# Optimization experiments

Measured on AMD Instinct MI355X. Metric: run time of the kernel, lower is better.

Reference implementation:

```python
import jax, jax.numpy as jnp
import numpy as np

H = 8        # hidden_size
T = 609      # seq_size
IN = 5       # input feature dim
B = 2048     # batch


def _lstm_layer(x, Wih, Whh, bih, bhh):
    """PyTorch-compatible single-layer LSTM, batch_first. x: [B, T, I].
    Gate order i, f, g, o; zero initial (h, c)."""
    b = x.shape[0]
    h_dim = Wih.shape[0] // 4
    bias = bih + bhh

    def step(carry, xt):
        h, c = carry
        gates = xt @ Wih.T + h @ Whh.T + bias          # [B, 4H]
        i, f, g, o = jnp.split(gates, 4, axis=-1)
        i = jax.nn.sigmoid(i)
        f = jax.nn.sigmoid(f)
        g = jnp.tanh(g)
        o = jax.nn.sigmoid(o)
        c = f * c + i * g
        h = o * jnp.tanh(c)
        return (h, c), h

    h0 = jnp.zeros((b, h_dim), x.dtype)
    (_, _), ys = jax.lax.scan(step, (h0, h0), jnp.swapaxes(x, 0, 1))  # ys: [T, B, H]
    return jnp.swapaxes(ys, 0, 1)                                      # [B, T, H]


def setup_inputs() -> dict:
    key = jax.random.key(0)
    ks = jax.random.split(key, 20)
    s_lstm = 1.0 / np.sqrt(H)   # PyTorch LSTM init scale

    def u(k, shape, s):
        return jax.random.uniform(k, shape, jnp.float32, -s, s)

    inp = {"x": jax.random.normal(ks[0], (B, T, IN), jnp.float32)}
    # LSTM layer 1 (input 5), layers 2-3 (input H)
    ins = [IN, H, H]
    for l in range(3):
        k0, k1, k2, k3 = jax.random.split(ks[1 + l], 4)
        inp[f"Wih{l+1}"] = u(k0, (4 * H, ins[l]), s_lstm)
        inp[f"Whh{l+1}"] = u(k1, (4 * H, H), s_lstm)
        inp[f"bih{l+1}"] = u(k2, (4 * H,), s_lstm)
        inp[f"bhh{l+1}"] = u(k3, (4 * H,), s_lstm)
    # MLP head
    d_in = H * T  # 4872
    dims = [(4096, d_in), (1024, 4096), (T, 1024)]
    for i, (o, ii) in enumerate(dims):
        s = 1.0 / np.sqrt(ii)
        k0, k1 = jax.random.split(ks[10 + i], 2)
        inp[f"W{i+1}"] = u(k0, (o, ii), s)
        inp[f"b{i+1}"] = u(k1, (o,), s)
    return inp


def reference(x, Wih1, Whh1, bih1, bhh1, Wih2, Whh2, bih2, bhh2,
              Wih3, Whh3, bih3, bhh3, W1, b1, W2, b2, W3, b3):
    out = _lstm_layer(x, Wih1, Whh1, bih1, bhh1)
    out = _lstm_layer(out, Wih2, Whh2, bih2, bhh2)
    out = _lstm_layer(out, Wih3, Whh3, bih3, bhh3)
    out = out.reshape(x.shape[0], -1)              # [B, T*H]
    out = jax.nn.relu(out @ W1.T + b1)
    out = jax.nn.relu(out @ W2.T + b2)
    out = out @ W3.T + b3                          # [B, T]
    return out
```

## Files before the change

kernel.cpp:

```cpp
#include <hip/hip_runtime.h>
#include <hip/hip_bf16.h>

typedef __attribute__((ext_vector_type(8))) short short8;
typedef __attribute__((ext_vector_type(4))) float floatx4;
typedef unsigned short u16;

#define T_SZ 609
#define K1V  4872
#define K1P  4928
#define RD   4

static __device__ __forceinline__ u16 f2bf(float f) {
    union { float f; unsigned u; } a; a.f = f;
    unsigned r = a.u + 0x7FFF + ((a.u >> 16) & 1);
    return (u16)(r >> 16);
}

static __device__ __forceinline__ void gload_lds16(const u16* g, u16* l) {
    __builtin_amdgcn_global_load_lds(
        (const __attribute__((address_space(1))) void*)g,
        (__attribute__((address_space(3))) void*)l, 16, 0, 0);
}

#define WG_LOAD(p)     __hip_atomic_load((p), __ATOMIC_ACQUIRE, __HIP_MEMORY_SCOPE_WORKGROUP)
#define WG_STORE(p, v) __hip_atomic_store((p), (v), __ATOMIC_RELEASE, __HIP_MEMORY_SCOPE_WORKGROUP)

static __device__ __forceinline__ void cvt8(const float* __restrict__ p, u16* __restrict__ d) {
    float4 a = *(const float4*)p;
    float4 b = *(const float4*)(p + 4);
    u16 o[8] = { f2bf(a.x), f2bf(a.y), f2bf(a.z), f2bf(a.w),
                 f2bf(b.x), f2bf(b.y), f2bf(b.z), f2bf(b.w) };
    *(uint4*)d = *(const uint4*)o;
}
static __device__ __forceinline__ void zero8(u16* __restrict__ d) {
    *(uint4*)d = (uint4){0, 0, 0, 0};
}

__global__ __launch_bounds__(192) void lstm3_fused(
    const float* __restrict__ x,
    const float* __restrict__ Wih1, const float* __restrict__ Whh1,
    const float* __restrict__ bih1, const float* __restrict__ bhh1,
    const float* __restrict__ Wih2, const float* __restrict__ Whh2,
    const float* __restrict__ bih2, const float* __restrict__ bhh2,
    const float* __restrict__ Wih3, const float* __restrict__ Whh3,
    const float* __restrict__ bih3, const float* __restrict__ bhh3,
    u16* __restrict__ A1,
    const float* __restrict__ W1, u16* __restrict__ W1b,
    const float* __restrict__ W2, u16* __restrict__ W2b,
    const float* __restrict__ W3, u16* __restrict__ W3b)
{
    if (blockIdx.x >= 1024) {
        const int ct = (blockIdx.x - 1024) * 192 + threadIdx.x;
        const int cs = 256 * 192;
        for (int i = ct; i < 4096 * 616; i += cs) {
            int r = i / 616, c = (i - r * 616) << 3;
            u16* d = W1b + (size_t)r * K1P + c;
            if (c < K1V) cvt8(W1 + (size_t)r * K1V + c, d); else zero8(d);
        }
        for (int i = ct; i < 524288; i += cs)
            cvt8(W2 + (size_t)i * 8, W2b + (size_t)i * 8);
        for (int i = ct; i < 640 * 128; i += cs) {
            int r = i >> 7, c = (i & 127) << 3;
            u16* d = W3b + (size_t)r * 1024 + c;
            if (r < T_SZ) cvt8(W3 + (size_t)r * 1024 + c, d); else zero8(d);
        }
        return;
    }

    __shared__ __align__(16) float xs[2 * T_SZ * 5];
    __shared__ __align__(16) float r1[RD * 16], r2[RD * 16], r3[RD * 16];
    __shared__ int p1, p2, c2, c3;

    const int tid = threadIdx.x;
    const int b0  = blockIdx.x * 2;

    const float* xg = x + (size_t)b0 * (T_SZ * 5);
    for (int i = tid; i < 2 * T_SZ * 5; i += 192) xs[i] = xg[i];
    if (tid == 0) { p1 = 0; p2 = 0; c2 = 0; c3 = 0; }
    if (tid < 112) {
        int r = tid / 56, c = tid - r * 56;
        A1[(size_t)(b0 + r) * K1P + K1V + c] = 0;
    }
    __syncthreads();

    const int lane = tid & 63, wid = tid >> 6;
    const int gi   = lane & 31;
    const int rh   = lane >> 5;
    const int jj   = gi & 7;
    const int gt   = gi >> 3;
    const int base = lane & 32;

    const float am = (gt == 2) ? -2.f : -1.f;
    const float aa = (gt == 2) ?  2.f :  1.f;
    const float ab = (gt == 2) ? -1.f :  0.f;

    auto lstep = [&](float a, float& c) -> float {
        float e = __expf(am * a);
        float v = __builtin_fmaf(aa, __fdividef(1.f, 1.f + e), ab);
        float vi = __shfl(v, base + jj,      64);
        float vf = __shfl(v, base + 8 + jj,  64);
        float vg = __shfl(v, base + 16 + jj, 64);
        float vo = __shfl(v, base + 24 + jj, 64);
        c = __builtin_fmaf(vf, c, vi * vg);
        float ec = __expf(-2.f * __builtin_fabsf(c));
        float th = (1.f - ec) * __fdividef(1.f, 1.f + ec);
        return vo * __builtin_copysignf(th, c);
    };

    auto dot8 = [&](const float* hp, const float* w, float& a, float& b) {
        float4 h0 = *(const float4*)hp;
        float4 h1 = *(const float4*)(hp + 4);
        a = __builtin_fmaf(w[0], h0.x, a); b = __builtin_fmaf(w[1], h0.y, b);
        a = __builtin_fmaf(w[2], h0.z, a); b = __builtin_fmaf(w[3], h0.w, b);
        a = __builtin_fmaf(w[4], h1.x, a); b = __builtin_fmaf(w[5], h1.y, b);
        a = __builtin_fmaf(w[6], h1.z, a); b = __builtin_fmaf(w[7], h1.w, b);
    };

    if (wid == 0) {
        float wi[5], wh[8];
#pragma unroll
        for (int k = 0; k < 5; ++k) wi[k] = Wih1[gi * 5 + k];
#pragma unroll
        for (int k = 0; k < 8; ++k) wh[k] = Whh1[gi * 8 + k];
        const float bs = bih1[gi] + bhh1[gi];
        const float* xr = &xs[rh * (T_SZ * 5)];
        float cst = 0.f;
        for (int t = 0; t < T_SZ; ++t) {
            float a = bs, b = 0.f;
#pragma unroll
            for (int k = 0; k < 5; ++k) a = __builtin_fmaf(wi[k], xr[t * 5 + k], a);
            if (t > 0) dot8(&r1[((t - 1) & (RD - 1)) * 16 + rh * 8], wh, a, b);
            float h = lstep(a + b, cst);
            if (t >= RD) while (WG_LOAD(&c2) < t - (RD - 1)) {}
            if (gi < 8) r1[(t & (RD - 1)) * 16 + rh * 8 + jj] = h;
            if (lane == 0) WG_STORE(&p1, t + 1);
        }
    } else if (wid == 1) {
        float wi[8], wh[8];
#pragma unroll
        for (int k = 0; k < 8; ++k) { wi[k] = Wih2[gi * 8 + k]; wh[k] = Whh2[gi * 8 + k]; }
        const float bs = bih2[gi] + bhh2[gi];
        float cst = 0.f;
        for (int t = 0; t < T_SZ; ++t) {
            while (WG_LOAD(&p1) < t + 1) {}
            float a = bs, b = 0.f;
            dot8(&r1[(t & (RD - 1)) * 16 + rh * 8], wi, a, b);
            if (lane == 0) WG_STORE(&c2, t + 1);
            if (t > 0) dot8(&r2[((t - 1) & (RD - 1)) * 16 + rh * 8], wh, a, b);
            float h = lstep(a + b, cst);
            if (t >= RD) while (WG_LOAD(&c3) < t - (RD - 1)) {}
            if (gi < 8) r2[(t & (RD - 1)) * 16 + rh * 8 + jj] = h;
            if (lane == 0) WG_STORE(&p2, t + 1);
        }
    } else {
        float wi[8], wh[8];
#pragma unroll
        for (int k = 0; k < 8; ++k) { wi[k] = Wih3[gi * 8 + k]; wh[k] = Whh3[gi * 8 + k]; }
        const float bs = bih3[gi] + bhh3[gi];
        float cst = 0.f;
        u16* outp = A1 + (size_t)(b0 + rh) * K1P;
        for (int t = 0; t < T_SZ; ++t) {
            while (WG_LOAD(&p2) < t + 1) {}
            float a = bs, b = 0.f;
            dot8(&r2[(t & (RD - 1)) * 16 + rh * 8], wi, a, b);
            if (lane == 0) WG_STORE(&c3, t + 1);
            if (t > 0) dot8(&r3[((t - 1) & (RD - 1)) * 16 + rh * 8], wh, a, b);
            float h = lstep(a + b, cst);
            if (gi < 8) {
                r3[(t & (RD - 1)) * 16 + rh * 8 + jj] = h;
                outp[t * 8 + jj] = f2bf(h);
            }
        }
    }
}

template<int BM, int BN, bool RELU, bool NGUARD, bool OUTF32>
__global__ __launch_bounds__(256) void gemm_bt(
    const u16* __restrict__ A, int lda,
    const u16* __restrict__ B, int ldb,
    const float* __restrict__ bias,
    void* __restrict__ Cv, int ldc, int N, int K)
{
    constexpr int WM = BM / 2, WN = BN / 2;
    constexpr int TM = WM / 16, TN = WN / 16;
    __shared__ u16 As[BM * 64];
    __shared__ u16 Bs[BN * 64];

    const int tid = threadIdx.x;
    const int bm  = blockIdx.y * BM;
    const int bn  = blockIdx.x * BN;
    const int l   = tid & 63, w = tid >> 6;
    const int wr  = w >> 1, wc = w & 1;
    const int lr  = l & 15, q = l >> 4;
    const int lrow = l >> 3;
    const int lcol = (l & 7) << 3;

    floatx4 acc[TM][TN];
#pragma unroll
    for (int i = 0; i < TM; ++i)
#pragma unroll
        for (int j = 0; j < TN; ++j) acc[i][j] = (floatx4){0.f, 0.f, 0.f, 0.f};

    const u16* Ab = A + (size_t)bm * lda;
    const u16* Bb = B + (size_t)bn * ldb;

    for (int k0 = 0; k0 < K; k0 += 64) {
#pragma unroll
        for (int i = 0; i < BM / 32; ++i) {
            int r0 = w * (BM / 4) + i * 8;
            gload_lds16(Ab + (size_t)(r0 + lrow) * lda + k0 + lcol, &As[r0 * 64]);
        }
#pragma unroll
        for (int i = 0; i < BN / 32; ++i) {
            int r0 = w * (BN / 4) + i * 8;
            gload_lds16(Bb + (size_t)(r0 + lrow) * ldb + k0 + lcol, &Bs[r0 * 64]);
        }
        __syncthreads();

#pragma unroll
        for (int ks = 0; ks < 2; ++ks) {
            short8 fa[TM], fb[TN];
#pragma unroll
            for (int i = 0; i < TM; ++i)
                fa[i] = *(const short8*)&As[(wr * WM + i * 16 + lr) * 64 + ks * 32 + q * 8];
#pragma unroll
            for (int j = 0; j < TN; ++j)
                fb[j] = *(const short8*)&Bs[(wc * WN + j * 16 + lr) * 64 + ks * 32 + q * 8];
#pragma unroll
            for (int i = 0; i < TM; ++i)
#pragma unroll
                for (int j = 0; j < TN; ++j)
                    acc[i][j] = __builtin_amdgcn_mfma_f32_16x16x32_bf16(fa[i], fb[j], acc[i][j], 0, 0, 0);
        }
        __syncthreads();
    }

#pragma unroll
    for (int j = 0; j < TN; ++j) {
        int n = bn + wc * WN + j * 16 + lr;
        bool nok = (!NGUARD) || (n < N);
        float bv = nok ? bias[n] : 0.f;
#pragma unroll
        for (int i = 0; i < TM; ++i) {
            int m0r = bm + wr * WM + i * 16 + q * 4;
#pragma unroll
            for (int r = 0; r < 4; ++r) {
                float vv = acc[i][j][r] + bv;
                if (RELU) vv = fmaxf(vv, 0.f);
                if (nok) {
                    size_t idx = (size_t)(m0r + r) * ldc + n;
                    if (OUTF32) ((float*)Cv)[idx] = vv;
                    else        ((u16*)Cv)[idx] = f2bf(vv);
                }
            }
        }
    }
}

extern "C" void kernel_launch(void* const* d_in, const int* in_sizes, int n_in,
                              void* d_out, int out_size, void* d_ws, size_t ws_size,
                              hipStream_t stream)
{
    const float* x    = (const float*)d_in[0];
    const float* Wih1 = (const float*)d_in[1];
    const float* Whh1 = (const float*)d_in[2];
    const float* bih1 = (const float*)d_in[3];
    const float* bhh1 = (const float*)d_in[4];
    const float* Wih2 = (const float*)d_in[5];
    const float* Whh2 = (const float*)d_in[6];
    const float* bih2 = (const float*)d_in[7];
    const float* bhh2 = (const float*)d_in[8];
    const float* Wih3 = (const float*)d_in[9];
    const float* Whh3 = (const float*)d_in[10];
    const float* bih3 = (const float*)d_in[11];
    const float* bhh3 = (const float*)d_in[12];
    const float* W1 = (const float*)d_in[13];
    const float* b1 = (const float*)d_in[14];
    const float* W2 = (const float*)d_in[15];
    const float* b2 = (const float*)d_in[16];
    const float* W3 = (const float*)d_in[17];
    const float* b3 = (const float*)d_in[18];

    u16* A1  = (u16*)d_ws;
    u16* A2  = A1  + (size_t)2048 * K1P;
    u16* A3  = A2  + (size_t)2048 * 4096;
    u16* W1b = A3  + (size_t)2048 * 1024;
    u16* W2b = W1b + (size_t)4096 * K1P;
    u16* W3b = W2b + (size_t)1024 * 4096;

    lstm3_fused<<<1280, 192, 0, stream>>>(x, Wih1, Whh1, bih1, bhh1,
                                          Wih2, Whh2, bih2, bhh2,
                                          Wih3, Whh3, bih3, bhh3, A1,
                                          W1, W1b, W2, W2b, W3, W3b);

    gemm_bt<128, 128, true, false, false><<<dim3(32, 16), 256, 0, stream>>>(
        A1, K1P, W1b, K1P, b1, A2, 4096, 4096, K1P);

    gemm_bt<64, 128, true, false, false><<<dim3(8, 32), 256, 0, stream>>>(
        A2, 4096, W2b, 4096, b2, A3, 1024, 1024, 4096);

    gemm_bt<64, 64, false, true, true><<<dim3(10, 32), 256, 0, stream>>>(
        A3, 1024, W3b, 1024, b3, d_out, T_SZ, T_SZ, 1024);
}
```

Measured before the change: 641.7 us.

## Process two LSTM timesteps per handshake and deepen ring buffer to 8

Each of the three wavefront-pipelined LSTM layers now computes two timesteps between progress-flag updates, which halves the number of cross-wave spin-wait and atomic store operations. The LDS ring buffer depth grows from 4 to 8 slots, and the back-pressure checks move to the start of each step pair. The second GEMM also switches to 64x64 tiles with twice as many blocks. In exchange, the downstream layer waits for a pair of steps before it can start, so the pipeline stages overlap at a coarser grain.

```diff
diff --git a/kernel.cpp b/kernel.cpp
--- a/kernel.cpp
+++ b/kernel.cpp
@@ -8,7 +8,7 @@
 #define T_SZ 609
 #define K1V  4872
 #define K1P  4928
-#define RD   4
+#define RD   8
 
 static __device__ __forceinline__ u16 f2bf(float f) {
     union { float f; unsigned u; } a; a.f = f;
@@ -125,15 +125,32 @@
         const float bs = bih1[gi] + bhh1[gi];
         const float* xr = &xs[rh * (T_SZ * 5)];
         float cst = 0.f;
-        for (int t = 0; t < T_SZ; ++t) {
+        for (int t0 = 0; t0 < T_SZ - 1; t0 += 2) {
+            while (WG_LOAD(&c2) < t0 - 6) {}
+            float a = bs, b = 0.f;
+#pragma unroll
+            for (int k = 0; k < 5; ++k) a = __builtin_fmaf(wi[k], xr[t0 * 5 + k], a);
+            if (t0 > 0) dot8(&r1[((t0 - 1) & 7) * 16 + rh * 8], wh, a, b);
+            float h = lstep(a + b, cst);
+            if (gi < 8) r1[(t0 & 7) * 16 + rh * 8 + jj] = h;
+            float a2 = bs, b2 = 0.f;
+#pragma unroll
+            for (int k = 0; k < 5; ++k) a2 = __builtin_fmaf(wi[k], xr[(t0 + 1) * 5 + k], a2);
+            dot8(&r1[(t0 & 7) * 16 + rh * 8], wh, a2, b2);
+            float h2 = lstep(a2 + b2, cst);
+            if (gi < 8) r1[((t0 + 1) & 7) * 16 + rh * 8 + jj] = h2;
+            if (lane == 0) WG_STORE(&p1, t0 + 2);
+        }
+        {
+            const int t = T_SZ - 1;
+            while (WG_LOAD(&c2) < t - 6) {}
             float a = bs, b = 0.f;
 #pragma unroll
             for (int k = 0; k < 5; ++k) a = __builtin_fmaf(wi[k], xr[t * 5 + k], a);
-            if (t > 0) dot8(&r1[((t - 1) & (RD - 1)) * 16 + rh * 8], wh, a, b);
-            float h = lstep(a + b, cst);
-            if (t >= RD) while (WG_LOAD(&c2) < t - (RD - 1)) {}
-            if (gi < 8) r1[(t & (RD - 1)) * 16 + rh * 8 + jj] = h;
-            if (lane == 0) WG_STORE(&p1, t + 1);
+            dot8(&r1[((t - 1) & 7) * 16 + rh * 8], wh, a, b);
+            float h = lstep(a + b, cst);
+            if (gi < 8) r1[(t & 7) * 16 + rh * 8 + jj] = h;
+            if (lane == 0) WG_STORE(&p1, T_SZ);
         }
     } else if (wid == 1) {
         float wi[8], wh[8];
@@ -141,16 +158,33 @@
         for (int k = 0; k < 8; ++k) { wi[k] = Wih2[gi * 8 + k]; wh[k] = Whh2[gi * 8 + k]; }
         const float bs = bih2[gi] + bhh2[gi];
         float cst = 0.f;
-        for (int t = 0; t < T_SZ; ++t) {
-            while (WG_LOAD(&p1) < t + 1) {}
-            float a = bs, b = 0.f;
-            dot8(&r1[(t & (RD - 1)) * 16 + rh * 8], wi, a, b);
-            if (lane == 0) WG_STORE(&c2, t + 1);
-            if (t > 0) dot8(&r2[((t - 1) & (RD - 1)) * 16 + rh * 8], wh, a, b);
-            float h = lstep(a + b, cst);
-            if (t >= RD) while (WG_LOAD(&c3) < t - (RD - 1)) {}
-            if (gi < 8) r2[(t & (RD - 1)) * 16 + rh * 8 + jj] = h;
-            if (lane == 0) WG_STORE(&p2, t + 1);
+        for (int t0 = 0; t0 < T_SZ - 1; t0 += 2) {
+            while (WG_LOAD(&p1) < t0 + 2) {}
+            while (WG_LOAD(&c3) < t0 - 6) {}
+            float a = bs, b = 0.f;
+            dot8(&r1[(t0 & 7) * 16 + rh * 8], wi, a, b);
+            float a2 = bs, b2 = 0.f;
+            dot8(&r1[((t0 + 1) & 7) * 16 + rh * 8], wi, a2, b2);
+            if (lane == 0) WG_STORE(&c2, t0 + 2);
+            if (t0 > 0) dot8(&r2[((t0 - 1) & 7) * 16 + rh * 8], wh, a, b);
+            float h = lstep(a + b, cst);
+            if (gi < 8) r2[(t0 & 7) * 16 + rh * 8 + jj] = h;
+            dot8(&r2[(t0 & 7) * 16 + rh * 8], wh, a2, b2);
+            float h2 = lstep(a2 + b2, cst);
+            if (gi < 8) r2[((t0 + 1) & 7) * 16 + rh * 8 + jj] = h2;
+            if (lane == 0) WG_STORE(&p2, t0 + 2);
+        }
+        {
+            const int t = T_SZ - 1;
+            while (WG_LOAD(&p1) < T_SZ) {}
+            while (WG_LOAD(&c3) < t - 6) {}
+            float a = bs, b = 0.f;
+            dot8(&r1[(t & 7) * 16 + rh * 8], wi, a, b);
+            if (lane == 0) WG_STORE(&c2, T_SZ);
+            dot8(&r2[((t - 1) & 7) * 16 + rh * 8], wh, a, b);
+            float h = lstep(a + b, cst);
+            if (gi < 8) r2[(t & 7) * 16 + rh * 8 + jj] = h;
+            if (lane == 0) WG_STORE(&p2, T_SZ);
         }
     } else {
         float wi[8], wh[8];
@@ -159,17 +193,35 @@
         const float bs = bih3[gi] + bhh3[gi];
         float cst = 0.f;
         u16* outp = A1 + (size_t)(b0 + rh) * K1P;
-        for (int t = 0; t < T_SZ; ++t) {
-            while (WG_LOAD(&p2) < t + 1) {}
-            float a = bs, b = 0.f;
-            dot8(&r2[(t & (RD - 1)) * 16 + rh * 8], wi, a, b);
-            if (lane == 0) WG_STORE(&c3, t + 1);
-            if (t > 0) dot8(&r3[((t - 1) & (RD - 1)) * 16 + rh * 8], wh, a, b);
+        for (int t0 = 0; t0 < T_SZ - 1; t0 += 2) {
+            while (WG_LOAD(&p2) < t0 + 2) {}
+            float a = bs, b = 0.f;
+            dot8(&r2[(t0 & 7) * 16 + rh * 8], wi, a, b);
+            float a2 = bs, b2 = 0.f;
+            dot8(&r2[((t0 + 1) & 7) * 16 + rh * 8], wi, a2, b2);
+            if (lane == 0) WG_STORE(&c3, t0 + 2);
+            if (t0 > 0) dot8(&r3[((t0 - 1) & 7) * 16 + rh * 8], wh, a, b);
             float h = lstep(a + b, cst);
             if (gi < 8) {
-                r3[(t & (RD - 1)) * 16 + rh * 8 + jj] = h;
-                outp[t * 8 + jj] = f2bf(h);
+                r3[(t0 & 7) * 16 + rh * 8 + jj] = h;
+                outp[t0 * 8 + jj] = f2bf(h);
             }
+            dot8(&r3[(t0 & 7) * 16 + rh * 8], wh, a2, b2);
+            float h2 = lstep(a2 + b2, cst);
+            if (gi < 8) {
+                r3[((t0 + 1) & 7) * 16 + rh * 8 + jj] = h2;
+                outp[(t0 + 1) * 8 + jj] = f2bf(h2);
+            }
+        }
+        {
+            const int t = T_SZ - 1;
+            while (WG_LOAD(&p2) < T_SZ) {}
+            float a = bs, b = 0.f;
+            dot8(&r2[(t & 7) * 16 + rh * 8], wi, a, b);
+            if (lane == 0) WG_STORE(&c3, T_SZ);
+            dot8(&r3[((t - 1) & 7) * 16 + rh * 8], wh, a, b);
+            float h = lstep(a + b, cst);
+            if (gi < 8) outp[t * 8 + jj] = f2bf(h);
         }
     }
 }
@@ -296,7 +348,7 @@
     gemm_bt<128, 128, true, false, false><<<dim3(32, 16), 256, 0, stream>>>(
         A1, K1P, W1b, K1P, b1, A2, 4096, 4096, K1P);
 
-    gemm_bt<64, 128, true, false, false><<<dim3(8, 32), 256, 0, stream>>>(
+    gemm_bt<64, 64, true, false, false><<<dim3(16, 32), 256, 0, stream>>>(
         A2, 4096, W2b, 4096, b2, A3, 1024, 1024, 4096);
 
     gemm_bt<64, 64, false, true, true><<<dim3(10, 32), 256, 0, stream>>>(
```

New measurement: 597.7 us. 1.07x faster.
